# Performance work log

Measured on AMD Instinct MI355X. Metric: run time of the kernel, lower is better.

The kernel has to match this reference:

```python
import jax, jax.numpy as jnp
import numpy as np

N_NODES = 50000
N_EDGES = 600000
NUM_RELS = 5
IN_CH = 768
HID = 128
OUT_CH = 128
REL_DIM = 200


def _segment_softmax(scores, seg, n):
    # numerically stable softmax over variable-size segments (destination nodes)
    m = jax.ops.segment_max(scores, seg, num_segments=n)
    e = jnp.exp(scores - m[seg])
    s = jax.ops.segment_sum(e, seg, num_segments=n)
    return e / s[seg]


def _hgn_conv(x, edge_index, edge_type, W, Wr, a, Wres, rel_tab, final):
    # x: [N, h_in]; W: [h, h_in]; Wr: [h, rel_dim]; a: [3h]; rel_tab: [R, rel_dim]
    src = edge_index[0]
    dst = edge_index[1]
    n = x.shape[0]
    h = W.shape[0]
    Wx = x @ W.T                      # [N, h] (shared by x_i, x_j, messages)
    rel = rel_tab[edge_type] @ Wr.T   # [E, h]
    aA, aB, aC = a[:h], a[h:2 * h], a[2 * h:]
    # a([Wx_i | Wx_j | Wr rel]) decomposed to avoid materializing the concat
    score = Wx[dst] @ aA + Wx[src] @ aB + rel @ aC   # [E]
    alpha = jax.nn.leaky_relu(score, 0.2)
    alpha = _segment_softmax(alpha, dst, n)
    agg = jax.ops.segment_sum(Wx[src] * alpha[:, None], dst, num_segments=n)
    out = jax.nn.elu(agg + x @ Wres.T)
    if final:
        out = out / jnp.maximum(jnp.linalg.norm(out, axis=1, keepdims=True), 1e-12)
    return out, alpha


def setup_inputs() -> dict:
    key = jax.random.key(0)
    ks = jax.random.split(key, 20)
    s = 0.02
    return {
        "x": jax.random.normal(ks[0], (N_NODES, IN_CH), jnp.float32),
        "edge_index": jax.random.randint(ks[1], (2, N_EDGES), 0, N_NODES, jnp.int64 if jax.config.jax_enable_x64 else jnp.int32),
        "edge_type": jax.random.randint(ks[2], (N_EDGES,), 0, NUM_RELS, jnp.int64 if jax.config.jax_enable_x64 else jnp.int32),
        "l1_W": jax.random.normal(ks[3], (HID, IN_CH), jnp.float32) * s,
        "l1_b": jnp.zeros((HID,), jnp.float32),
        "l2_W": jax.random.normal(ks[4], (OUT_CH, HID), jnp.float32) * s,
        "l2_b": jnp.zeros((OUT_CH,), jnp.float32),
        "W1": jax.random.normal(ks[5], (HID, HID), jnp.float32) * s,
        "Wr1": jax.random.normal(ks[6], (HID, REL_DIM), jnp.float32) * s,
        "a1": jax.random.normal(ks[7], (3 * HID,), jnp.float32) * s,
        "Wres1": jax.random.normal(ks[8], (HID, HID), jnp.float32) * s,
        "rel1": jax.random.normal(ks[9], (NUM_RELS, REL_DIM), jnp.float32),
        "W2": jax.random.normal(ks[10], (HID, HID), jnp.float32) * s,
        "Wr2": jax.random.normal(ks[11], (HID, REL_DIM), jnp.float32) * s,
        "a2": jax.random.normal(ks[12], (3 * HID,), jnp.float32) * s,
        "Wres2": jax.random.normal(ks[13], (HID, HID), jnp.float32) * s,
        "rel2": jax.random.normal(ks[14], (NUM_RELS, REL_DIM), jnp.float32),
    }


def reference(x, edge_index, edge_type, l1_W, l1_b, l2_W, l2_b,
              W1, Wr1, a1, Wres1, rel1, W2, Wr2, a2, Wres2, rel2):
    out = jax.nn.leaky_relu(x @ l1_W.T + l1_b, 0.01)
    # layer 1 (dropout is identity in eval mode)
    out, alpha = _hgn_conv(out, edge_index, edge_type, W1, Wr1, a1, Wres1, rel1, final=False)
    # layer 2: original code blends alpha into self.alpha but weights messages
    # with its own (unblended) softmax alpha, so pre_alpha does not affect output
    out, _ = _hgn_conv(out, edge_index, edge_type, W2, Wr2, a2, Wres2, rel2, final=True)
    out = jax.nn.leaky_relu(out @ l2_W.T + l2_b, 0.01)
    return out
```

## Files before the change

kernel.cpp:

```cpp
#include <hip/hip_runtime.h>

namespace {

typedef unsigned short ushort_t;
typedef unsigned int uint_t;
typedef __attribute__((ext_vector_type(8))) short bf16x8;
typedef __attribute__((ext_vector_type(4))) float f32x4;

constexpr int N   = 50000;
constexpr int E   = 600000;
constexpr int NR  = 5;
constexpr int KIN = 768;
constexpr int H   = 128;
constexpr int RD  = 200;

__device__ inline ushort_t f2b(float f){
  uint_t u = __builtin_bit_cast(uint_t, f);
  uint_t r = (u + 0x7FFFu + ((u >> 16) & 1u)) >> 16;
  return (ushort_t)r;
}
__device__ inline float b2f_lo(uint_t u){ return __builtin_bit_cast(float, u << 16); }
__device__ inline float b2f_hi(uint_t u){ return __builtin_bit_cast(float, u & 0xFFFF0000u); }
__device__ inline float b2f_us(ushort_t h){ return __builtin_bit_cast(float, ((uint_t)h) << 16); }

__global__ void prep_k(const float* __restrict__ l1W, const float* __restrict__ W1,
                       const float* __restrict__ R1, const float* __restrict__ W2,
                       const float* __restrict__ R2, const float* __restrict__ l2W,
                       ushort_t* __restrict__ wts, int* __restrict__ deg,
                       const float* __restrict__ rel1, const float* __restrict__ Wr1,
                       const float* __restrict__ a1, float* __restrict__ sC1,
                       const float* __restrict__ rel2, const float* __restrict__ Wr2,
                       const float* __restrict__ a2, float* __restrict__ sC2){
  constexpr int S0 = H * KIN;
  constexpr int S1 = H * H;
  int b = blockIdx.x, tid = threadIdx.x;
  if (b < 704){
    int i = b * 256 + tid;
    float v;
    if (i < S0) v = l1W[i];
    else {
      int j = i - S0, seg = j >> 14, off = j & (S1 - 1);
      const float* srcs[5] = {W1, R1, W2, R2, l2W};
      v = srcs[seg][off];
    }
    wts[i] = f2b(v);
  } else if (b < 900){
    int i = (b - 704) * 256 + tid;
    if (i < N) deg[i] = 0;
  } else {
    int L = b - 900;
    const float* rel = L ? rel2 : rel1;
    const float* Wr  = L ? Wr2  : Wr1;
    const float* a   = L ? a2   : a1;
    float*       sC  = L ? sC2  : sC1;
    __shared__ float red[256];
    int n = tid >> 1, half = tid & 1;
    float aC = a[256 + n];
    for (int r = 0; r < NR; ++r){
      float p = 0.f;
      for (int k = half * 100; k < half * 100 + 100; ++k)
        p += rel[r * RD + k] * Wr[n * RD + k];
      red[tid] = p * aC;
      __syncthreads();
      for (int s = 128; s > 0; s >>= 1){
        if (tid < s) red[tid] += red[tid + s];
        __syncthreads();
      }
      if (tid == 0) sC[r] = red[0];
      __syncthreads();
    }
  }
}

__global__ void degcount_k(const int* __restrict__ dst, int* __restrict__ deg){
  int e = blockIdx.x * 256 + threadIdx.x;
  if (e < E) atomicAdd(&deg[dst[e]], 1);
}

__global__ void scan1_k(const int* __restrict__ deg, int* __restrict__ chunk,
                        int* __restrict__ bsums, int n){
  __shared__ int s[256];
  int tid = threadIdx.x, i = blockIdx.x * 256 + tid;
  int v = (i < n) ? deg[i] : 0;
  s[tid] = v; __syncthreads();
  for (int off = 1; off < 256; off <<= 1){
    int t = (tid >= off) ? s[tid - off] : 0;
    __syncthreads();
    s[tid] += t;
    __syncthreads();
  }
  if (i < n) chunk[i] = s[tid] - v;
  if (tid == 255) bsums[blockIdx.x] = s[255];
}

__global__ void scan2_k(const int* __restrict__ bsums, int* __restrict__ boffs, int nb){
  __shared__ int s[256];
  int tid = threadIdx.x;
  int v = (tid < nb) ? bsums[tid] : 0;
  s[tid] = v; __syncthreads();
  for (int off = 1; off < 256; off <<= 1){
    int t = (tid >= off) ? s[tid - off] : 0;
    __syncthreads();
    s[tid] += t;
    __syncthreads();
  }
  if (tid < nb) boffs[tid] = s[tid] - v;
}

__global__ void scan3_k(int* __restrict__ rowptr, const int* __restrict__ boffs,
                        int* __restrict__ cursor, int n, int total){
  int i = blockIdx.x * 256 + threadIdx.x;
  if (i < n){
    int v = rowptr[i] + boffs[blockIdx.x];
    rowptr[i] = v; cursor[i] = v;
  }
  if (i == 0) rowptr[n] = total;
}

__global__ void fill_k(const int* __restrict__ src, const int* __restrict__ dst,
                       const int* __restrict__ et, int* __restrict__ cursor,
                       int* __restrict__ cpk){
  int e = blockIdx.x * 256 + threadIdx.x;
  if (e < E){
    int d = dst[e];
    int p = atomicAdd(&cursor[d], 1);
    cpk[p] = src[e] | (et[e] << 16);
  }
}

template<int K1, int M1, bool AFP32, bool NORM, bool STORE1, int M2>
__global__ __launch_bounds__(256) void gfused_k(
    const void* __restrict__ Ap, const ushort_t* __restrict__ Wb1,
    const float* __restrict__ bias1, const ushort_t* __restrict__ aggM,
    ushort_t* __restrict__ out1,
    const ushort_t* __restrict__ Wb2, const float* __restrict__ vec2,
    void* __restrict__ out2, float* __restrict__ sA, float* __restrict__ sB, int M)
{
  constexpr int AP = 40;
  constexpr int BP = 40;
  constexpr int CP = 136;
  __shared__ __align__(16) ushort_t As[64 * AP];
  __shared__ __align__(16) ushort_t Bs[128 * BP];
  __shared__ __align__(16) ushort_t Cs[64 * CP];
  const int tid  = threadIdx.x;
  const int wave = tid >> 6, lane = tid & 63;
  const int l15  = lane & 15, quad = lane >> 4;
  const int row0 = blockIdx.x * 64;

  if (M1 == 2){
    #pragma unroll
    for (int i = 0; i < 4; ++i){
      int idx = tid + 256 * i;
      int r = idx >> 4, c8 = idx & 15;
      int grow = row0 + r;
      uint4 v = make_uint4(0, 0, 0, 0);
      if (grow < M) v = *reinterpret_cast<const uint4*>(aggM + (size_t)grow * 128 + c8 * 8);
      *reinterpret_cast<uint4*>(&Cs[r * CP + c8 * 8]) = v;
    }
  }

  f32x4 acc[8];
  #pragma unroll
  for (int t = 0; t < 8; ++t) acc[t] = (f32x4){0.f, 0.f, 0.f, 0.f};

  for (int k0 = 0; k0 < K1; k0 += 32){
    {
      int r = tid >> 2, q = tid & 3;
      int grow = row0 + r;
      ushort_t v[8] = {0,0,0,0,0,0,0,0};
      if (grow < M){
        if (AFP32){
          const float* ap = (const float*)Ap + (size_t)grow * K1 + k0 + q * 8;
          float4 u0 = *reinterpret_cast<const float4*>(ap);
          float4 u1 = *reinterpret_cast<const float4*>(ap + 4);
          v[0]=f2b(u0.x); v[1]=f2b(u0.y); v[2]=f2b(u0.z); v[3]=f2b(u0.w);
          v[4]=f2b(u1.x); v[5]=f2b(u1.y); v[6]=f2b(u1.z); v[7]=f2b(u1.w);
        } else {
          const uint4 u = *reinterpret_cast<const uint4*>(
              (const ushort_t*)Ap + (size_t)grow * K1 + k0 + q * 8);
          *reinterpret_cast<uint4*>(v) = u;
        }
      }
      *reinterpret_cast<uint4*>(&As[r * AP + q * 8]) = *reinterpret_cast<uint4*>(v);
    }
    {
      int n = tid >> 1, seg = tid & 1;
      const ushort_t* wp = Wb1 + (size_t)n * K1 + k0 + seg * 16;
      uint4 v0 = *reinterpret_cast<const uint4*>(wp);
      uint4 v1 = *reinterpret_cast<const uint4*>(wp + 8);
      *reinterpret_cast<uint4*>(&Bs[n * BP + seg * 16])     = v0;
      *reinterpret_cast<uint4*>(&Bs[n * BP + seg * 16 + 8]) = v1;
    }
    __syncthreads();
    bf16x8 af = *reinterpret_cast<const bf16x8*>(&As[(wave * 16 + l15) * AP + quad * 8]);
    #pragma unroll
    for (int t = 0; t < 8; ++t){
      bf16x8 bfr = *reinterpret_cast<const bf16x8*>(&Bs[(t * 16 + l15) * BP + quad * 8]);
      acc[t] = __builtin_amdgcn_mfma_f32_16x16x32_bf16(af, bfr, acc[t], 0, 0, 0);
    }
    __syncthreads();
  }

  float vv[8][4];
  #pragma unroll
  for (int t = 0; t < 8; ++t){
    #pragma unroll
    for (int r = 0; r < 4; ++r){
      int lr  = wave * 16 + quad * 4 + r;
      int col = t * 16 + l15;
      float v = acc[t][r];
      if (M1 == 1){
        v += bias1[col];
        v = v > 0.f ? v : 0.01f * v;
      } else {
        v += b2f_us(Cs[lr * CP + col]);
        v = v > 0.f ? v : __expf(v) - 1.f;
      }
      vv[t][r] = v;
    }
  }
  if (NORM){
    #pragma unroll
    for (int r = 0; r < 4; ++r){
      float ss = 0.f;
      #pragma unroll
      for (int t = 0; t < 8; ++t) ss += vv[t][r] * vv[t][r];
      #pragma unroll
      for (int off = 1; off < 16; off <<= 1) ss += __shfl_xor(ss, off, 64);
      float sc = 1.f / fmaxf(sqrtf(ss), 1e-12f);
      #pragma unroll
      for (int t = 0; t < 8; ++t) vv[t][r] *= sc;
    }
  }
  #pragma unroll
  for (int t = 0; t < 8; ++t){
    #pragma unroll
    for (int r = 0; r < 4; ++r){
      int lr  = wave * 16 + quad * 4 + r;
      int col = t * 16 + l15;
      int grow = row0 + lr;
      ushort_t h = f2b(vv[t][r]);
      if (STORE1 && grow < M) out1[(size_t)grow * 128 + col] = h;
      Cs[lr * CP + col] = h;
    }
  }
  __syncthreads();

  #pragma unroll
  for (int t = 0; t < 8; ++t) acc[t] = (f32x4){0.f, 0.f, 0.f, 0.f};
  for (int k0 = 0; k0 < 128; k0 += 32){
    {
      int n = tid >> 1, seg = tid & 1;
      const ushort_t* wp = Wb2 + (size_t)n * 128 + k0 + seg * 16;
      uint4 v0 = *reinterpret_cast<const uint4*>(wp);
      uint4 v1 = *reinterpret_cast<const uint4*>(wp + 8);
      *reinterpret_cast<uint4*>(&Bs[n * BP + seg * 16])     = v0;
      *reinterpret_cast<uint4*>(&Bs[n * BP + seg * 16 + 8]) = v1;
    }
    __syncthreads();
    bf16x8 af = *reinterpret_cast<const bf16x8*>(&Cs[(wave * 16 + l15) * CP + k0 + quad * 8]);
    #pragma unroll
    for (int t = 0; t < 8; ++t){
      bf16x8 bfr = *reinterpret_cast<const bf16x8*>(&Bs[(t * 16 + l15) * BP + quad * 8]);
      acc[t] = __builtin_amdgcn_mfma_f32_16x16x32_bf16(af, bfr, acc[t], 0, 0, 0);
    }
    __syncthreads();
  }

  if (M2 == 1){
    #pragma unroll
    for (int t = 0; t < 8; ++t){
      #pragma unroll
      for (int r = 0; r < 4; ++r){
        int grow = row0 + wave * 16 + quad * 4 + r;
        if (grow >= M) continue;
        int col = t * 16 + l15;
        float v = acc[t][r] + vec2[col];
        v = v > 0.f ? v : 0.01f * v;
        ((float*)out2)[(size_t)grow * 128 + col] = v;
      }
    }
  } else {
    #pragma unroll
    for (int t = 0; t < 8; ++t){
      #pragma unroll
      for (int r = 0; r < 4; ++r){
        int grow = row0 + wave * 16 + quad * 4 + r;
        if (grow >= M) continue;
        int col = t * 16 + l15;
        ((ushort_t*)out2)[(size_t)grow * 128 + col] = f2b(acc[t][r]);
      }
    }
    #pragma unroll
    for (int r = 0; r < 4; ++r){
      float pa = 0.f, pb = 0.f;
      #pragma unroll
      for (int t = 0; t < 8; ++t){
        int col = t * 16 + l15;
        pa += acc[t][r] * vec2[col];
        pb += acc[t][r] * vec2[128 + col];
      }
      #pragma unroll
      for (int off = 1; off < 16; off <<= 1){
        pa += __shfl_xor(pa, off, 64);
        pb += __shfl_xor(pb, off, 64);
      }
      int grow = row0 + wave * 16 + quad * 4 + r;
      if (l15 == r && grow < M){ sA[grow] = pa; sB[grow] = pb; }
    }
  }
}

__global__ void agg_k(const ushort_t* __restrict__ Wx, const float* __restrict__ sA,
                      const float* __restrict__ sB, const float* __restrict__ sC,
                      const int* __restrict__ rowptr, const int* __restrict__ cpk,
                      uint_t* __restrict__ aggU, int n){
  int node = blockIdx.x * 4 + (threadIdx.x >> 6);
  int lane = threadIdx.x & 63;
  if (node >= n) return;
  int p0 = rowptr[node], p1 = rowptr[node + 1];
  int deg = p1 - p0;
  float sa = sA[node];
  float m = -1e30f, ssum = 0.f, a0 = 0.f, a1 = 0.f;

  for (int c0 = 0; c0 < deg; c0 += 64){
    int cnt = deg - c0; if (cnt > 64) cnt = 64;
    bool ok = lane < cnt;
    int p  = p0 + c0 + (ok ? lane : 0);
    int pk = cpk[p];
    int sn = pk & 0xFFFF;
    float s = sa + sB[sn] + sC[pk >> 16];
    s = s > 0.f ? s : 0.2f * s;
    float sv = ok ? s : -1e30f;
    #pragma unroll
    for (int off = 32; off > 0; off >>= 1) sv = fmaxf(sv, __shfl_xor(sv, off, 64));
    float mn = fmaxf(m, sv);
    float corr = __expf(m - mn);
    ssum *= corr; a0 *= corr; a1 *= corr;
    float ev = ok ? __expf(s - mn) : 0.f;
    float es = ev;
    #pragma unroll
    for (int off = 32; off > 0; off >>= 1) es += __shfl_xor(es, off, 64);
    ssum += es;
    int png = ok ? pk : 0;
    m = mn;

    for (int e = 0; e < cnt; e += 4){
      int  n0 = __shfl(png, e,     64) & 0xFFFF, n1 = __shfl(png, e + 1, 64) & 0xFFFF;
      int  n2 = __shfl(png, e + 2, 64) & 0xFFFF, n3 = __shfl(png, e + 3, 64) & 0xFFFF;
      float e0 = __shfl(ev, e,     64), e1 = __shfl(ev, e + 1, 64);
      float e2 = __shfl(ev, e + 2, 64), e3 = __shfl(ev, e + 3, 64);
      uint_t u0 = *reinterpret_cast<const uint_t*>(Wx + (size_t)n0 * 128 + lane * 2);
      uint_t u1 = *reinterpret_cast<const uint_t*>(Wx + (size_t)n1 * 128 + lane * 2);
      uint_t u2 = *reinterpret_cast<const uint_t*>(Wx + (size_t)n2 * 128 + lane * 2);
      uint_t u3 = *reinterpret_cast<const uint_t*>(Wx + (size_t)n3 * 128 + lane * 2);
      a0 += e0 * b2f_lo(u0); a1 += e0 * b2f_hi(u0);
      a0 += e1 * b2f_lo(u1); a1 += e1 * b2f_hi(u1);
      a0 += e2 * b2f_lo(u2); a1 += e2 * b2f_hi(u2);
      a0 += e3 * b2f_lo(u3); a1 += e3 * b2f_hi(u3);
    }
  }
  float inv = (deg > 0) ? 1.f / ssum : 0.f;
  uint_t o = (uint_t)f2b(a0 * inv) | ((uint_t)f2b(a1 * inv) << 16);
  aggU[(size_t)node * 64 + lane] = o;
}

}

extern "C" void kernel_launch(void* const* d_in, const int* in_sizes, int n_in,
                              void* d_out, int out_size, void* d_ws, size_t ws_size,
                              hipStream_t stream)
{
  const float* x     = (const float*)d_in[0];
  const int*   eidx  = (const int*)d_in[1];
  const int*   et    = (const int*)d_in[2];
  const float* l1W   = (const float*)d_in[3];
  const float* l1b   = (const float*)d_in[4];
  const float* l2W   = (const float*)d_in[5];
  const float* l2b   = (const float*)d_in[6];
  const float* W1    = (const float*)d_in[7];
  const float* Wr1   = (const float*)d_in[8];
  const float* a1    = (const float*)d_in[9];
  const float* Wres1 = (const float*)d_in[10];
  const float* rel1  = (const float*)d_in[11];
  const float* W2    = (const float*)d_in[12];
  const float* Wr2   = (const float*)d_in[13];
  const float* a2    = (const float*)d_in[14];
  const float* Wres2 = (const float*)d_in[15];
  const float* rel2  = (const float*)d_in[16];
  float* outp = (float*)d_out;

  const int* esrc = eidx;
  const int* edst = eidx + E;

  float* f = (float*)d_ws;
  size_t o = 0;
  float* sA   = f + o; o += N;
  float* sB   = f + o; o += N;
  float* sC1  = f + o; o += 8;
  float* sC2  = f + o; o += 8;
  ushort_t* us = (ushort_t*)(f + o);
  size_t ou = 0;
  ushort_t* b0   = us + ou; ou += (size_t)N * H;
  ushort_t* b1   = us + ou; ou += (size_t)N * H;
  ushort_t* Wxb  = us + ou; ou += (size_t)N * H;
  ushort_t* aggB = us + ou; ou += (size_t)N * H;
  ushort_t* wtsb = us + ou; ou += (size_t)H * KIN + 5 * H * H;
  ushort_t* l1Wb = wtsb;
  ushort_t* W1b  = wtsb + H * KIN;
  ushort_t* R1b  = W1b + H * H;
  ushort_t* W2b  = R1b + H * H;
  ushort_t* R2b  = W2b + H * H;
  ushort_t* l2Wb = R2b + H * H;
  if (ou & 1) ou += 1;
  int* wi = (int*)(us + ou);
  size_t oi = 0;
  int* deg    = wi + oi; oi += N;
  int* rowptr = wi + oi; oi += N + 1;
  int* cursor = wi + oi; oi += N;
  int* bsums  = wi + oi; oi += 256;
  int* boffs  = wi + oi; oi += 256;
  int* cpk    = wi + oi; oi += E;

  const int EB    = (E + 255) / 256;
  const int NB256 = (N + 255) / 256;
  const int GB    = (N + 63) / 64;
  const int NB4   = (N + 3) / 4;

  prep_k<<<902, 256, 0, stream>>>(l1W, W1, Wres1, W2, Wres2, l2W, wtsb, deg,
                                  rel1, Wr1, a1, sC1, rel2, Wr2, a2, sC2);
  degcount_k<<<EB, 256, 0, stream>>>(edst, deg);
  scan1_k<<<NB256, 256, 0, stream>>>(deg, rowptr, bsums, N);
  scan2_k<<<1, 256, 0, stream>>>(bsums, boffs, NB256);
  scan3_k<<<NB256, 256, 0, stream>>>(rowptr, boffs, cursor, N, E);
  fill_k<<<EB, 256, 0, stream>>>(esrc, edst, et, cursor, cpk);

  gfused_k<KIN, 1, true, false, true, 3><<<GB, 256, 0, stream>>>(
      x, l1Wb, l1b, nullptr, b0, W1b, a1, Wxb, sA, sB, N);
  agg_k<<<NB4, 256, 0, stream>>>(Wxb, sA, sB, sC1, rowptr, cpk, (uint_t*)aggB, N);

  gfused_k<H, 2, false, false, true, 3><<<GB, 256, 0, stream>>>(
      b0, R1b, nullptr, aggB, b1, W2b, a2, Wxb, sA, sB, N);
  agg_k<<<NB4, 256, 0, stream>>>(Wxb, sA, sB, sC2, rowptr, cpk, (uint_t*)aggB, N);

  gfused_k<H, 2, false, true, false, 1><<<GB, 256, 0, stream>>>(
      b1, R2b, nullptr, aggB, nullptr, l2Wb, l2b, outp, nullptr, nullptr, N);
}
```

Before: 483.3 us.

## Use 16-lane groups per node in aggregation and prefetch GEMM tiles

The aggregation kernel now assigns 16 lanes per destination node instead of a full 64-lane wave. Each lane loads 16-byte vectors and keeps 8 accumulators, which cuts idle lanes on low-degree nodes (about 12 edges on average). The fused GEMM kernel prefetches the next K-slice into registers while the current one is computed. It also loads the whole second weight matrix into shared memory once, removing per-step barriers, and uses the hardware packed bf16 conversion instruction. Shared memory use grows and register pressure rises from the prefetch and weight staging.

```diff
diff --git a/kernel.cpp b/kernel.cpp
--- a/kernel.cpp
+++ b/kernel.cpp
@@ -22,6 +22,11 @@
 __device__ inline float b2f_lo(uint_t u){ return __builtin_bit_cast(float, u << 16); }
 __device__ inline float b2f_hi(uint_t u){ return __builtin_bit_cast(float, u & 0xFFFF0000u); }
 __device__ inline float b2f_us(ushort_t h){ return __builtin_bit_cast(float, ((uint_t)h) << 16); }
+__device__ inline uint_t cvtpk(float lo, float hi){
+  uint_t r;
+  asm("v_cvt_pk_bf16_f32 %0, %1, %2" : "=v"(r) : "v"(lo), "v"(hi));
+  return r;
+}
 
 __global__ void prep_k(const float* __restrict__ l1W, const float* __restrict__ W1,
                        const float* __restrict__ R1, const float* __restrict__ W2,
@@ -139,9 +144,11 @@
   constexpr int AP = 40;
   constexpr int BP = 40;
   constexpr int CP = 136;
-  __shared__ __align__(16) ushort_t As[64 * AP];
-  __shared__ __align__(16) ushort_t Bs[128 * BP];
+  __shared__ __align__(16) ushort_t U[128 * CP];
   __shared__ __align__(16) ushort_t Cs[64 * CP];
+  ushort_t* const As  = U;
+  ushort_t* const Bs  = U + 64 * AP;
+  ushort_t* const B2s = U;
   const int tid  = threadIdx.x;
   const int wave = tid >> 6, lane = tid & 63;
   const int l15  = lane & 15, quad = lane >> 4;
@@ -163,35 +170,55 @@
   #pragma unroll
   for (int t = 0; t < 8; ++t) acc[t] = (f32x4){0.f, 0.f, 0.f, 0.f};
 
+  const int ar = tid >> 2, aq = tid & 3;
+  const int agrow = row0 + ar;
+  const bool aok = agrow < M;
+  const int bn = tid >> 1, bs16 = (tid & 1) * 16;
+
+  float4 pf0 = make_float4(0.f, 0.f, 0.f, 0.f), pf1 = pf0;
+  uint4  pu  = make_uint4(0, 0, 0, 0);
+  uint4  pb0, pb1;
+
+  if (AFP32){
+    if (aok){
+      const float* ap = (const float*)Ap + (size_t)agrow * K1 + aq * 8;
+      pf0 = *reinterpret_cast<const float4*>(ap);
+      pf1 = *reinterpret_cast<const float4*>(ap + 4);
+    }
+  } else if (aok){
+    pu = *reinterpret_cast<const uint4*>((const ushort_t*)Ap + (size_t)agrow * K1 + aq * 8);
+  }
+  {
+    const ushort_t* wp = Wb1 + (size_t)bn * K1 + bs16;
+    pb0 = *reinterpret_cast<const uint4*>(wp);
+    pb1 = *reinterpret_cast<const uint4*>(wp + 8);
+  }
+
   for (int k0 = 0; k0 < K1; k0 += 32){
-    {
-      int r = tid >> 2, q = tid & 3;
-      int grow = row0 + r;
-      ushort_t v[8] = {0,0,0,0,0,0,0,0};
-      if (grow < M){
-        if (AFP32){
-          const float* ap = (const float*)Ap + (size_t)grow * K1 + k0 + q * 8;
-          float4 u0 = *reinterpret_cast<const float4*>(ap);
-          float4 u1 = *reinterpret_cast<const float4*>(ap + 4);
-          v[0]=f2b(u0.x); v[1]=f2b(u0.y); v[2]=f2b(u0.z); v[3]=f2b(u0.w);
-          v[4]=f2b(u1.x); v[5]=f2b(u1.y); v[6]=f2b(u1.z); v[7]=f2b(u1.w);
-        } else {
-          const uint4 u = *reinterpret_cast<const uint4*>(
-              (const ushort_t*)Ap + (size_t)grow * K1 + k0 + q * 8);
-          *reinterpret_cast<uint4*>(v) = u;
+    uint4 av;
+    if (AFP32){
+      av.x = cvtpk(pf0.x, pf0.y); av.y = cvtpk(pf0.z, pf0.w);
+      av.z = cvtpk(pf1.x, pf1.y); av.w = cvtpk(pf1.z, pf1.w);
+    } else av = pu;
+    *reinterpret_cast<uint4*>(&As[ar * AP + aq * 8]) = av;
+    *reinterpret_cast<uint4*>(&Bs[bn * BP + bs16])     = pb0;
+    *reinterpret_cast<uint4*>(&Bs[bn * BP + bs16 + 8]) = pb1;
+    __syncthreads();
+    if (k0 + 32 < K1){
+      const int k1 = k0 + 32;
+      if (AFP32){
+        if (aok){
+          const float* ap = (const float*)Ap + (size_t)agrow * K1 + k1 + aq * 8;
+          pf0 = *reinterpret_cast<const float4*>(ap);
+          pf1 = *reinterpret_cast<const float4*>(ap + 4);
         }
-      }
-      *reinterpret_cast<uint4*>(&As[r * AP + q * 8]) = *reinterpret_cast<uint4*>(v);
-    }
-    {
-      int n = tid >> 1, seg = tid & 1;
-      const ushort_t* wp = Wb1 + (size_t)n * K1 + k0 + seg * 16;
-      uint4 v0 = *reinterpret_cast<const uint4*>(wp);
-      uint4 v1 = *reinterpret_cast<const uint4*>(wp + 8);
-      *reinterpret_cast<uint4*>(&Bs[n * BP + seg * 16])     = v0;
-      *reinterpret_cast<uint4*>(&Bs[n * BP + seg * 16 + 8]) = v1;
-    }
-    __syncthreads();
+      } else if (aok){
+        pu = *reinterpret_cast<const uint4*>((const ushort_t*)Ap + (size_t)agrow * K1 + k1 + aq * 8);
+      }
+      const ushort_t* wp = Wb1 + (size_t)bn * K1 + k1 + bs16;
+      pb0 = *reinterpret_cast<const uint4*>(wp);
+      pb1 = *reinterpret_cast<const uint4*>(wp + 8);
+    }
     bf16x8 af = *reinterpret_cast<const bf16x8*>(&As[(wave * 16 + l15) * AP + quad * 8]);
     #pragma unroll
     for (int t = 0; t < 8; ++t){
@@ -199,6 +226,14 @@
       acc[t] = __builtin_amdgcn_mfma_f32_16x16x32_bf16(af, bfr, acc[t], 0, 0, 0);
     }
     __syncthreads();
+  }
+
+  uint4 wreg[8];
+  #pragma unroll
+  for (int i = 0; i < 8; ++i){
+    int idx = tid + 256 * i;
+    int rr = idx >> 4, c8 = idx & 15;
+    wreg[i] = *reinterpret_cast<const uint4*>(Wb2 + (size_t)rr * 128 + c8 * 8);
   }
 
   float vv[8][4];
@@ -219,6 +254,12 @@
       vv[t][r] = v;
     }
   }
+  #pragma unroll
+  for (int i = 0; i < 8; ++i){
+    int idx = tid + 256 * i;
+    int rr = idx >> 4, c8 = idx & 15;
+    *reinterpret_cast<uint4*>(&B2s[rr * CP + c8 * 8]) = wreg[i];
+  }
   if (NORM){
     #pragma unroll
     for (int r = 0; r < 4; ++r){
@@ -233,38 +274,35 @@
     }
   }
   #pragma unroll
-  for (int t = 0; t < 8; ++t){
+  for (int t = 0; t < 8; t += 2){
     #pragma unroll
     for (int r = 0; r < 4; ++r){
       int lr  = wave * 16 + quad * 4 + r;
-      int col = t * 16 + l15;
-      int grow = row0 + lr;
-      ushort_t h = f2b(vv[t][r]);
-      if (STORE1 && grow < M) out1[(size_t)grow * 128 + col] = h;
-      Cs[lr * CP + col] = h;
+      int c0  = t * 16 + l15, c1 = c0 + 16;
+      uint_t pr = cvtpk(vv[t][r], vv[t + 1][r]);
+      Cs[lr * CP + c0] = (ushort_t)pr;
+      Cs[lr * CP + c1] = (ushort_t)(pr >> 16);
+      if (STORE1){
+        int grow = row0 + lr;
+        if (grow < M){
+          out1[(size_t)grow * 128 + c0] = (ushort_t)pr;
+          out1[(size_t)grow * 128 + c1] = (ushort_t)(pr >> 16);
+        }
+      }
     }
   }
   __syncthreads();
 
   #pragma unroll
   for (int t = 0; t < 8; ++t) acc[t] = (f32x4){0.f, 0.f, 0.f, 0.f};
-  for (int k0 = 0; k0 < 128; k0 += 32){
-    {
-      int n = tid >> 1, seg = tid & 1;
-      const ushort_t* wp = Wb2 + (size_t)n * 128 + k0 + seg * 16;
-      uint4 v0 = *reinterpret_cast<const uint4*>(wp);
-      uint4 v1 = *reinterpret_cast<const uint4*>(wp + 8);
-      *reinterpret_cast<uint4*>(&Bs[n * BP + seg * 16])     = v0;
-      *reinterpret_cast<uint4*>(&Bs[n * BP + seg * 16 + 8]) = v1;
-    }
-    __syncthreads();
-    bf16x8 af = *reinterpret_cast<const bf16x8*>(&Cs[(wave * 16 + l15) * CP + k0 + quad * 8]);
+  #pragma unroll
+  for (int kk = 0; kk < 4; ++kk){
+    bf16x8 af2 = *reinterpret_cast<const bf16x8*>(&Cs[(wave * 16 + l15) * CP + kk * 32 + quad * 8]);
     #pragma unroll
     for (int t = 0; t < 8; ++t){
-      bf16x8 bfr = *reinterpret_cast<const bf16x8*>(&Bs[(t * 16 + l15) * BP + quad * 8]);
-      acc[t] = __builtin_amdgcn_mfma_f32_16x16x32_bf16(af, bfr, acc[t], 0, 0, 0);
-    }
-    __syncthreads();
+      bf16x8 bfr = *reinterpret_cast<const bf16x8*>(&B2s[(t * 16 + l15) * CP + kk * 32 + quad * 8]);
+      acc[t] = __builtin_amdgcn_mfma_f32_16x16x32_bf16(af2, bfr, acc[t], 0, 0, 0);
+    }
   }
 
   if (M2 == 1){
@@ -282,13 +320,15 @@
     }
   } else {
     #pragma unroll
-    for (int t = 0; t < 8; ++t){
+    for (int t = 0; t < 8; t += 2){
       #pragma unroll
       for (int r = 0; r < 4; ++r){
         int grow = row0 + wave * 16 + quad * 4 + r;
         if (grow >= M) continue;
-        int col = t * 16 + l15;
-        ((ushort_t*)out2)[(size_t)grow * 128 + col] = f2b(acc[t][r]);
+        int c0 = t * 16 + l15;
+        uint_t pr = cvtpk(acc[t][r], acc[t + 1][r]);
+        ((ushort_t*)out2)[(size_t)grow * 128 + c0]      = (ushort_t)pr;
+        ((ushort_t*)out2)[(size_t)grow * 128 + c0 + 16] = (ushort_t)(pr >> 16);
       }
     }
     #pragma unroll
@@ -311,58 +351,81 @@
   }
 }
 
-__global__ void agg_k(const ushort_t* __restrict__ Wx, const float* __restrict__ sA,
-                      const float* __restrict__ sB, const float* __restrict__ sC,
-                      const int* __restrict__ rowptr, const int* __restrict__ cpk,
-                      uint_t* __restrict__ aggU, int n){
-  int node = blockIdx.x * 4 + (threadIdx.x >> 6);
-  int lane = threadIdx.x & 63;
+__global__ __launch_bounds__(256) void agg_k(
+    const ushort_t* __restrict__ Wx, const float* __restrict__ sA,
+    const float* __restrict__ sB, const float* __restrict__ sC,
+    const int* __restrict__ rowptr, const int* __restrict__ cpk,
+    uint_t* __restrict__ aggU, int n)
+{
+  const int node  = blockIdx.x * 16 + (threadIdx.x >> 4);
+  const int l     = threadIdx.x & 15;
+  const int gbase = threadIdx.x & 48;
   if (node >= n) return;
   int p0 = rowptr[node], p1 = rowptr[node + 1];
   int deg = p1 - p0;
   float sa = sA[node];
-  float m = -1e30f, ssum = 0.f, a0 = 0.f, a1 = 0.f;
-
-  for (int c0 = 0; c0 < deg; c0 += 64){
-    int cnt = deg - c0; if (cnt > 64) cnt = 64;
-    bool ok = lane < cnt;
-    int p  = p0 + c0 + (ok ? lane : 0);
-    int pk = cpk[p];
-    int sn = pk & 0xFFFF;
-    float s = sa + sB[sn] + sC[pk >> 16];
+  float m = -1e30f, ssum = 0.f;
+  float a[8];
+  #pragma unroll
+  for (int j = 0; j < 8; ++j) a[j] = 0.f;
+
+  for (int c0 = 0; c0 < deg; c0 += 16){
+    int cnt = deg - c0; if (cnt > 16) cnt = 16;
+    bool ok = l < cnt;
+    int pk = cpk[p0 + c0 + (ok ? l : 0)];
+    float s = sa + sB[pk & 0xFFFF] + sC[pk >> 16];
     s = s > 0.f ? s : 0.2f * s;
     float sv = ok ? s : -1e30f;
     #pragma unroll
-    for (int off = 32; off > 0; off >>= 1) sv = fmaxf(sv, __shfl_xor(sv, off, 64));
+    for (int off = 8; off > 0; off >>= 1) sv = fmaxf(sv, __shfl_xor(sv, off, 16));
     float mn = fmaxf(m, sv);
     float corr = __expf(m - mn);
-    ssum *= corr; a0 *= corr; a1 *= corr;
+    ssum *= corr;
+    #pragma unroll
+    for (int j = 0; j < 8; ++j) a[j] *= corr;
     float ev = ok ? __expf(s - mn) : 0.f;
     float es = ev;
     #pragma unroll
-    for (int off = 32; off > 0; off >>= 1) es += __shfl_xor(es, off, 64);
+    for (int off = 8; off > 0; off >>= 1) es += __shfl_xor(es, off, 16);
     ssum += es;
+    m = mn;
     int png = ok ? pk : 0;
-    m = mn;
 
     for (int e = 0; e < cnt; e += 4){
-      int  n0 = __shfl(png, e,     64) & 0xFFFF, n1 = __shfl(png, e + 1, 64) & 0xFFFF;
-      int  n2 = __shfl(png, e + 2, 64) & 0xFFFF, n3 = __shfl(png, e + 3, 64) & 0xFFFF;
-      float e0 = __shfl(ev, e,     64), e1 = __shfl(ev, e + 1, 64);
-      float e2 = __shfl(ev, e + 2, 64), e3 = __shfl(ev, e + 3, 64);
-      uint_t u0 = *reinterpret_cast<const uint_t*>(Wx + (size_t)n0 * 128 + lane * 2);
-      uint_t u1 = *reinterpret_cast<const uint_t*>(Wx + (size_t)n1 * 128 + lane * 2);
-      uint_t u2 = *reinterpret_cast<const uint_t*>(Wx + (size_t)n2 * 128 + lane * 2);
-      uint_t u3 = *reinterpret_cast<const uint_t*>(Wx + (size_t)n3 * 128 + lane * 2);
-      a0 += e0 * b2f_lo(u0); a1 += e0 * b2f_hi(u0);
-      a0 += e1 * b2f_lo(u1); a1 += e1 * b2f_hi(u1);
-      a0 += e2 * b2f_lo(u2); a1 += e2 * b2f_hi(u2);
-      a0 += e3 * b2f_lo(u3); a1 += e3 * b2f_hi(u3);
+      int b0l = gbase + e;
+      int pe0 = __shfl(png, b0l,     64), pe1 = __shfl(png, b0l + 1, 64);
+      int pe2 = __shfl(png, b0l + 2, 64), pe3 = __shfl(png, b0l + 3, 64);
+      float e0 = __shfl(ev, b0l,     64), e1 = __shfl(ev, b0l + 1, 64);
+      float e2 = __shfl(ev, b0l + 2, 64), e3 = __shfl(ev, b0l + 3, 64);
+      uint4 u0 = *reinterpret_cast<const uint4*>(Wx + (size_t)(pe0 & 0xFFFF) * 128 + l * 8);
+      uint4 u1 = *reinterpret_cast<const uint4*>(Wx + (size_t)(pe1 & 0xFFFF) * 128 + l * 8);
+      uint4 u2 = *reinterpret_cast<const uint4*>(Wx + (size_t)(pe2 & 0xFFFF) * 128 + l * 8);
+      uint4 u3 = *reinterpret_cast<const uint4*>(Wx + (size_t)(pe3 & 0xFFFF) * 128 + l * 8);
+      a[0] += e0 * b2f_lo(u0.x); a[1] += e0 * b2f_hi(u0.x);
+      a[2] += e0 * b2f_lo(u0.y); a[3] += e0 * b2f_hi(u0.y);
+      a[4] += e0 * b2f_lo(u0.z); a[5] += e0 * b2f_hi(u0.z);
+      a[6] += e0 * b2f_lo(u0.w); a[7] += e0 * b2f_hi(u0.w);
+      a[0] += e1 * b2f_lo(u1.x); a[1] += e1 * b2f_hi(u1.x);
+      a[2] += e1 * b2f_lo(u1.y); a[3] += e1 * b2f_hi(u1.y);
+      a[4] += e1 * b2f_lo(u1.z); a[5] += e1 * b2f_hi(u1.z);
+      a[6] += e1 * b2f_lo(u1.w); a[7] += e1 * b2f_hi(u1.w);
+      a[0] += e2 * b2f_lo(u2.x); a[1] += e2 * b2f_hi(u2.x);
+      a[2] += e2 * b2f_lo(u2.y); a[3] += e2 * b2f_hi(u2.y);
+      a[4] += e2 * b2f_lo(u2.z); a[5] += e2 * b2f_hi(u2.z);
+      a[6] += e2 * b2f_lo(u2.w); a[7] += e2 * b2f_hi(u2.w);
+      a[0] += e3 * b2f_lo(u3.x); a[1] += e3 * b2f_hi(u3.x);
+      a[2] += e3 * b2f_lo(u3.y); a[3] += e3 * b2f_hi(u3.y);
+      a[4] += e3 * b2f_lo(u3.z); a[5] += e3 * b2f_hi(u3.z);
+      a[6] += e3 * b2f_lo(u3.w); a[7] += e3 * b2f_hi(u3.w);
     }
   }
   float inv = (deg > 0) ? 1.f / ssum : 0.f;
-  uint_t o = (uint_t)f2b(a0 * inv) | ((uint_t)f2b(a1 * inv) << 16);
-  aggU[(size_t)node * 64 + lane] = o;
+  uint4 o;
+  o.x = cvtpk(a[0] * inv, a[1] * inv);
+  o.y = cvtpk(a[2] * inv, a[3] * inv);
+  o.z = cvtpk(a[4] * inv, a[5] * inv);
+  o.w = cvtpk(a[6] * inv, a[7] * inv);
+  *reinterpret_cast<uint4*>(aggU + (size_t)node * 64 + l * 4) = o;
 }
 
 }
@@ -425,7 +488,7 @@
   const int EB    = (E + 255) / 256;
   const int NB256 = (N + 255) / 256;
   const int GB    = (N + 63) / 64;
-  const int NB4   = (N + 3) / 4;
+  const int NB16  = (N + 15) / 16;
 
   prep_k<<<902, 256, 0, stream>>>(l1W, W1, Wres1, W2, Wres2, l2W, wtsb, deg,
                                   rel1, Wr1, a1, sC1, rel2, Wr2, a2, sC2);
@@ -437,11 +500,11 @@
 
   gfused_k<KIN, 1, true, false, true, 3><<<GB, 256, 0, stream>>>(
       x, l1Wb, l1b, nullptr, b0, W1b, a1, Wxb, sA, sB, N);
-  agg_k<<<NB4, 256, 0, stream>>>(Wxb, sA, sB, sC1, rowptr, cpk, (uint_t*)aggB, N);
+  agg_k<<<NB16, 256, 0, stream>>>(Wxb, sA, sB, sC1, rowptr, cpk, (uint_t*)aggB, N);
 
   gfused_k<H, 2, false, false, true, 3><<<GB, 256, 0, stream>>>(
       b0, R1b, nullptr, aggB, b1, W2b, a2, Wxb, sA, sB, N);
-  agg_k<<<NB4, 256, 0, stream>>>(Wxb, sA, sB, sC2, rowptr, cpk, (uint_t*)aggB, N);
+  agg_k<<<NB16, 256, 0, stream>>>(Wxb, sA, sB, sC2, rowptr, cpk, (uint_t*)aggB, N);
 
   gfused_k<H, 2, false, true, false, 1><<<GB, 256, 0, stream>>>(
       b1, R2b, nullptr, aggB, nullptr, l2Wb, l2b, outp, nullptr, nullptr, N);
```

After: 495.0 us. +2.4%, slower.
